# Performance work log

Measured on AMD Instinct MI355X. Metric: run time of the kernel, lower is better.

Reference implementation:

```python
import jax, jax.numpy as jnp
import numpy as np

N_NODES = 100000
N_EDGES = 1600000
F_IN = 128
HID = 128
N_GRAPHS = 64
G_FEAT = 16
N_CLASSES = 10


def _segment_softmax(e, seg, n):
    # numerically stable softmax over edges grouped by target node
    m = jax.ops.segment_max(e, seg, num_segments=n)
    ex = jnp.exp(e - m[seg])
    s = jax.ops.segment_sum(ex, seg, num_segments=n)
    return ex / s[seg]


def _gat_layer(x, src, dst, W, a_src, a_dst, b, n):
    # PyG GATConv (1 head): h = xW; e_ij = LeakyReLU(a_src.h_j + a_dst.h_i)
    h = x @ W                               # [N, H]
    es = h @ a_src                          # [N]
    ed = h @ a_dst                          # [N]
    e = jax.nn.leaky_relu(es[src] + ed[dst], negative_slope=0.2)  # [E]
    alpha = _segment_softmax(e, dst, n)     # softmax over incoming edges
    out = jax.ops.segment_sum(h[src] * alpha[:, None], dst, num_segments=n)
    return out + b


def setup_inputs() -> dict:
    key = jax.random.key(0)
    ks = jax.random.split(key, 16)
    x = jax.random.normal(ks[0], (N_NODES, F_IN), dtype=jnp.float32)
    edge_index = jax.random.randint(ks[1], (2, N_EDGES), 0, N_NODES)
    batch = jnp.sort(jax.random.randint(ks[2], (N_NODES,), 0, N_GRAPHS))
    graph_features = jax.random.normal(ks[3], (N_GRAPHS, G_FEAT), dtype=jnp.float32)
    s1 = 1.0 / np.sqrt(F_IN)
    s2 = 1.0 / np.sqrt(HID)
    params = dict(
        W1=jax.random.uniform(ks[4], (F_IN, HID), minval=-s1, maxval=s1),
        as1=jax.random.uniform(ks[5], (HID,), minval=-s2, maxval=s2),
        ad1=jax.random.uniform(ks[6], (HID,), minval=-s2, maxval=s2),
        b1=jnp.zeros((HID,), jnp.float32),
        W2=jax.random.uniform(ks[7], (HID, HID), minval=-s2, maxval=s2),
        as2=jax.random.uniform(ks[8], (HID,), minval=-s2, maxval=s2),
        ad2=jax.random.uniform(ks[9], (HID,), minval=-s2, maxval=s2),
        b2=jnp.zeros((HID,), jnp.float32),
        linW=jax.random.uniform(ks[10], (HID + G_FEAT, N_CLASSES), minval=-s2, maxval=s2),
        linb=jnp.zeros((N_CLASSES,), jnp.float32),
    )
    return dict(x=x, edge_index=edge_index, batch=batch,
                graph_features=graph_features, **params)


def reference(x, edge_index, batch, graph_features,
              W1, as1, ad1, b1, W2, as2, ad2, b2, linW, linb):
    n = x.shape[0]
    # add self loops (PyG GATConv default add_self_loops=True)
    loops = jnp.arange(n, dtype=edge_index.dtype)
    src = jnp.concatenate([edge_index[0], loops])
    dst = jnp.concatenate([edge_index[1], loops])

    h = jax.nn.relu(_gat_layer(x, src, dst, W1, as1, ad1, b1, n))
    h = jax.nn.relu(_gat_layer(h, src, dst, W2, as2, ad2, b2, n))

    # global_mean_pool over batch segments
    sums = jax.ops.segment_sum(h, batch, num_segments=N_GRAPHS)
    cnt = jax.ops.segment_sum(jnp.ones((n,), h.dtype), batch, num_segments=N_GRAPHS)
    pooled = sums / jnp.maximum(cnt, 1.0)[:, None]      # [G, H]
    # dropout(p=0.5) is identity at inference
    feat = jnp.concatenate([pooled, graph_features], axis=1)  # [G, H+G_FEAT]
    return feat @ linW + linb                           # [G, num_classes]
```

## Files before the change

kernel.cpp:

```cpp
#include <hip/hip_runtime.h>

#define WAVE 64
#define BUCKET_CAP 5632
#define NBUF 400
#define EPB 4096
#define PCHUNK 32

typedef __attribute__((ext_vector_type(8))) short short8v;
typedef __attribute__((ext_vector_type(4))) float floatx4;
typedef __attribute__((ext_vector_type(2))) float floatx2;

__device__ __forceinline__ ushort f2bf(float f) {
    union { float f; unsigned u; } v; v.f = f;
    unsigned r = v.u + 0x7FFF + ((v.u >> 16) & 1);
    return (ushort)(r >> 16);
}
__device__ __forceinline__ float bf2f(ushort u) {
    union { unsigned u; float f; } v; v.u = ((unsigned)u) << 16;
    return v.f;
}


__global__ void k_init(int* __restrict__ zreg, int nzero, int zblocks,
                       const float* __restrict__ W1, const float* __restrict__ W2,
                       ushort* __restrict__ T1, ushort* __restrict__ T2) {
    int b = blockIdx.x;
    if (b < zblocks) {
        int i = b * 256 + threadIdx.x;
        if (i < nzero) zreg[i] = 0;
    } else {
        const float* W = (b == zblocks) ? W1 : W2;
        ushort* T = (b == zblocks) ? T1 : T2;
        for (int i = threadIdx.x; i < 16384; i += 256) {
            int k = i >> 7, n = i & 127;
            T[n * 128 + k] = f2bf(W[k * 128 + n]);
        }
    }
}


__global__ __launch_bounds__(256) void k_bucket(const int* __restrict__ src,
                                                const int* __restrict__ dst,
                                                int E, int N, int B,
                                                int* __restrict__ bcnt,
                                                int* __restrict__ bucket) {
    __shared__ int cnt[NBUF];
    __shared__ int gbase[NBUF];
    int t = threadIdx.x;
    long base = (long)blockIdx.x * EPB;

    for (int k = t; k < NBUF; k += 256) cnt[k] = 0;
    __syncthreads();

    int pay[16], bk[16];
#pragma unroll
    for (int k = 0; k < 16; ++k) {
        long i = base + (long)k * 256 + t;
        bk[k] = -1;
        if (i < (long)E + N) {
            int d, s;
            if (i < E) { d = dst[i]; s = src[i]; }
            else       { d = (int)(i - E); s = d; }
            int b = d >> 8;
            bk[k] = b;
            pay[k] = ((d & 255) << 17) | s;
            atomicAdd(&cnt[b], 1);
        }
    }
    __syncthreads();

    for (int k = t; k < NBUF; k += 256) {
        int c = cnt[k];
        gbase[k] = (c > 0 && k < B) ? atomicAdd(&bcnt[k], c) : 0;
        cnt[k] = 0;
    }
    __syncthreads();

#pragma unroll
    for (int k = 0; k < 16; ++k) {
        if (bk[k] >= 0) {
            int lpos = atomicAdd(&cnt[bk[k]], 1);
            int pos = gbase[bk[k]] + lpos;
            if (pos < BUCKET_CAP)
                bucket[(size_t)bk[k] * BUCKET_CAP + pos] = pay[k];
        }
    }
}

__global__ void k_bscan(const int* __restrict__ bcnt, int* __restrict__ bbase,
                        int B, int Etot, int* __restrict__ offs, int N) {
    __shared__ int sh[512];
    int t = threadIdx.x;
    int v = (t < B) ? bcnt[t] : 0;
    sh[t] = v;
    __syncthreads();
    for (int o = 1; o < 512; o <<= 1) {
        int u = (t >= o) ? sh[t - o] : 0;
        __syncthreads();
        sh[t] += u;
        __syncthreads();
    }
    if (t < B) bbase[t] = sh[t] - v;
    if (t == 0) offs[N] = Etot;
}

__global__ __launch_bounds__(256) void k_csr(const int* __restrict__ bcnt,
                                             const int* __restrict__ bbase,
                                             const int* __restrict__ bucket,
                                             int* __restrict__ offs,
                                             int* __restrict__ csr, int N) {
    __shared__ int ebuf[BUCKET_CAP];
    __shared__ int cnt[256], sc[256], cur[256];
    int b = blockIdx.x, t = threadIdx.x;
    int n = bcnt[b]; if (n > BUCKET_CAP) n = BUCKET_CAP;
    int base = bbase[b];
    cnt[t] = 0;
    __syncthreads();
    const int* bk = bucket + (size_t)b * BUCKET_CAP;
    for (int k = t; k < n; k += 256) {
        int e = bk[k];
        ebuf[k] = e;
        atomicAdd(&cnt[e >> 17], 1);
    }
    __syncthreads();
    sc[t] = cnt[t];
    __syncthreads();
    for (int o = 1; o < 256; o <<= 1) {
        int u = (t >= o) ? sc[t - o] : 0;
        __syncthreads();
        sc[t] += u;
        __syncthreads();
    }
    int loff = sc[t] - cnt[t];
    int node = (b << 8) + t;
    if (node < N) offs[node] = base + loff;
    cur[t] = loff;
    __syncthreads();
    for (int k = t; k < n; k += 256) {
        int e = ebuf[k];
        int pos = base + atomicAdd(&cur[e >> 17], 1);
        csr[pos] = e & 0x1FFFF;
    }
}


template<bool AF32>
__global__ __launch_bounds__(256) void k_gemm_mfma(const void* __restrict__ Ain,
                                                   const ushort* __restrict__ Wt,
                                                   const float* __restrict__ a_s,
                                                   const float* __restrict__ a_d,
                                                   unsigned char* __restrict__ Cf8,
                                                   float* __restrict__ es,
                                                   float* __restrict__ ed, int M) {
    __shared__ ushort As[64][128];
    __shared__ ushort Ws[128][128];
    int t = threadIdx.x;
    int lane = t & 63, wid = t >> 6;
    int row0 = blockIdx.x * 64;

    {
        short8v w[8];
#pragma unroll
        for (int it = 0; it < 8; ++it) {
            int idx = it * 256 + t;
            w[it] = *(const short8v*)&Wt[(idx >> 4) * 128 + (idx & 15) * 8];
        }
#pragma unroll
        for (int it = 0; it < 8; ++it) {
            int idx = it * 256 + t;
            int r = idx >> 4, ch = idx & 15;
            *(short8v*)&Ws[r][(ch ^ (r & 15)) * 8] = w[it];
        }
    }
    {
        short8v a[4];
#pragma unroll
        for (int it = 0; it < 4; ++it) {
            int idx = it * 256 + t;
            int r = idx >> 4, ch = idx & 15;
            int gr = row0 + r;
            short8v u = {0, 0, 0, 0, 0, 0, 0, 0};
            if (gr < M) {
                if (AF32) {
                    const float* A = (const float*)Ain;
                    float4 f0 = *(const float4*)&A[(size_t)gr * 128 + ch * 8];
                    float4 f1 = *(const float4*)&A[(size_t)gr * 128 + ch * 8 + 4];
                    u[0] = (short)f2bf(f0.x); u[1] = (short)f2bf(f0.y);
                    u[2] = (short)f2bf(f0.z); u[3] = (short)f2bf(f0.w);
                    u[4] = (short)f2bf(f1.x); u[5] = (short)f2bf(f1.y);
                    u[6] = (short)f2bf(f1.z); u[7] = (short)f2bf(f1.w);
                } else {
                    const ushort* A = (const ushort*)Ain;
                    u = *(const short8v*)&A[(size_t)gr * 128 + ch * 8];
                }
            }
            a[it] = u;
        }
#pragma unroll
        for (int it = 0; it < 4; ++it) {
            int idx = it * 256 + t;
            int r = idx >> 4, ch = idx & 15;
            *(short8v*)&As[r][(ch ^ (r & 15)) * 8] = a[it];
        }
    }
    __syncthreads();

    int mrow = wid * 16;
    int col = lane & 15;
    int kg = lane >> 4;
    floatx4 acc[8] = {};

#pragma unroll
    for (int ks = 0; ks < 4; ++ks) {
        int chb = ks * 4 + kg;
        int r0 = mrow + col;
        short8v a0 = *(short8v*)&As[r0][(chb ^ (r0 & 15)) * 8];
        short8v b[8];
#pragma unroll
        for (int ni = 0; ni < 8; ++ni) {
            int rn = ni * 16 + col;
            b[ni] = *(short8v*)&Ws[rn][(chb ^ (rn & 15)) * 8];
        }
#pragma unroll
        for (int ni = 0; ni < 8; ++ni)
            acc[ni] = __builtin_amdgcn_mfma_f32_16x16x32_bf16(b[ni], a0, acc[ni], 0, 0, 0);
    }

    int node = row0 + mrow + col;
    bool ok = node < M;
    float esp = 0.f, edp = 0.f;
#pragma unroll
    for (int ni = 0; ni < 8; ++ni) {
        floatx4 v = acc[ni];
        float4 sv = *(const float4*)(a_s + ni * 16 + kg * 4);
        float4 dv = *(const float4*)(a_d + ni * 16 + kg * 4);
        esp += v[0] * sv.x + v[1] * sv.y + v[2] * sv.z + v[3] * sv.w;
        edp += v[0] * dv.x + v[1] * dv.y + v[2] * dv.z + v[3] * dv.w;
        int lo = __builtin_amdgcn_cvt_pk_fp8_f32(v[0], v[1], 0, false);
        int dw = __builtin_amdgcn_cvt_pk_fp8_f32(v[2], v[3], lo, true);
        if (ok) *(int*)&Cf8[(size_t)node * 128 + ni * 16 + kg * 4] = dw;
    }
    esp += __shfl_xor(esp, 16); esp += __shfl_xor(esp, 32);
    edp += __shfl_xor(edp, 16); edp += __shfl_xor(edp, 32);
    if (ok && kg == 0) { es[node] = esp; ed[node] = edp; }
}


__global__ __launch_bounds__(256) void k_aggregate(const unsigned char* __restrict__ hf8,
                                                   const float* __restrict__ es,
                                                   const float* __restrict__ ed,
                                                   const int* __restrict__ csr_src,
                                                   const int* __restrict__ offs,
                                                   const float* __restrict__ bias,
                                                   ushort* __restrict__ out, int N) {
    __shared__ __align__(16) float2 pe[4][64];
    int wid  = threadIdx.x >> 6;
    int lane = threadIdx.x & 63;
    int w = (blockIdx.x * 256 + threadIdx.x) >> 6;
    if (w >= N) return;
    int beg = offs[w], end = offs[w + 1];
    float edi = ed[w];
    int grp = lane >> 4, fc = lane & 15;
    const unsigned char* hbase = hf8 + fc * 8;

    float s_lane = 0.f;
    float acc[8] = {0.f, 0.f, 0.f, 0.f, 0.f, 0.f, 0.f, 0.f};

    for (int tb = beg; tb < end; tb += WAVE) {
        int cnt = end - tb; if (cnt > WAVE) cnt = WAVE;

        float p = 0.f;
        int sj = 0;
        if (lane < cnt) {
            sj = csr_src[tb + lane];
            float t = es[sj] + edi;
            float e = (t > 0.f) ? t : 0.2f * t;
            p = __expf(e);
        }
        s_lane += p;
        pe[wid][lane] = make_float2(p, __int_as_float(sj << 7));
        asm volatile("s_waitcnt lgkmcnt(0)" ::: "memory");

        __builtin_amdgcn_s_setprio(1);
        int cnt4 = (cnt + 3) & ~3;
        for (int k = 0; k < cnt4; k += 4) {
            float2 pr = pe[wid][k + grp];
            float p_ = pr.x;
            int off = __float_as_int(pr.y);
            uint2 v = *(const uint2*)(hbase + off);
            floatx2 f0 = __builtin_amdgcn_cvt_pk_f32_fp8(v.x, false);
            floatx2 f1 = __builtin_amdgcn_cvt_pk_f32_fp8(v.x, true);
            floatx2 f2 = __builtin_amdgcn_cvt_pk_f32_fp8(v.y, false);
            floatx2 f3 = __builtin_amdgcn_cvt_pk_f32_fp8(v.y, true);
            acc[0] += p_ * f0.x; acc[1] += p_ * f0.y;
            acc[2] += p_ * f1.x; acc[3] += p_ * f1.y;
            acc[4] += p_ * f2.x; acc[5] += p_ * f2.y;
            acc[6] += p_ * f3.x; acc[7] += p_ * f3.y;
        }
        __builtin_amdgcn_s_setprio(0);
    }

    float s = s_lane;
#pragma unroll
    for (int o = 32; o; o >>= 1) s += __shfl_xor(s, o);

#pragma unroll
    for (int i = 0; i < 8; ++i) {
        acc[i] += __shfl_xor(acc[i], 16);
        acc[i] += __shfl_xor(acc[i], 32);
    }

    if (grp == 0) {
        float rinv = 1.f / s;
        float4 b0 = *(const float4*)(bias + fc * 8);
        float4 b1 = *(const float4*)(bias + fc * 8 + 4);
        float o_[8];
        o_[0] = fmaxf(acc[0] * rinv + b0.x, 0.f);
        o_[1] = fmaxf(acc[1] * rinv + b0.y, 0.f);
        o_[2] = fmaxf(acc[2] * rinv + b0.z, 0.f);
        o_[3] = fmaxf(acc[3] * rinv + b0.w, 0.f);
        o_[4] = fmaxf(acc[4] * rinv + b1.x, 0.f);
        o_[5] = fmaxf(acc[5] * rinv + b1.y, 0.f);
        o_[6] = fmaxf(acc[6] * rinv + b1.z, 0.f);
        o_[7] = fmaxf(acc[7] * rinv + b1.w, 0.f);
        uint4 pk;
        pk.x = (unsigned)f2bf(o_[0]) | ((unsigned)f2bf(o_[1]) << 16);
        pk.y = (unsigned)f2bf(o_[2]) | ((unsigned)f2bf(o_[3]) << 16);
        pk.z = (unsigned)f2bf(o_[4]) | ((unsigned)f2bf(o_[5]) << 16);
        pk.w = (unsigned)f2bf(o_[6]) | ((unsigned)f2bf(o_[7]) << 16);
        *(uint4*)(out + (size_t)w * 128 + fc * 8) = pk;
    }
}


__global__ __launch_bounds__(128) void k_poolsum(const ushort* __restrict__ h,
                                                 const int* __restrict__ batch,
                                                 float* __restrict__ sums,
                                                 int* __restrict__ cnt, int N) {
    int t = threadIdx.x;
    int base = blockIdx.x * PCHUNK;
    if (base >= N) return;

    int cur = batch[base];
    float acc = 0.f;
    int cnum = 0;

    if (base + PCHUNK <= N) {
#pragma unroll
        for (int k = 0; k < PCHUNK; ++k) {
            int i = base + k;
            int g = batch[i];
            float v = bf2f(h[(size_t)i * 128 + t]);
            if (g != cur) {
                atomicAdd(&sums[cur * 128 + t], acc);
                if (t == 0) atomicAdd(&cnt[cur], cnum);
                acc = 0.f; cnum = 0; cur = g;
            }
            acc += v;
            ++cnum;
        }
    } else {
        for (int i = base; i < N; ++i) {
            int g = batch[i];
            float v = bf2f(h[(size_t)i * 128 + t]);
            if (g != cur) {
                atomicAdd(&sums[cur * 128 + t], acc);
                if (t == 0) atomicAdd(&cnt[cur], cnum);
                acc = 0.f; cnum = 0; cur = g;
            }
            acc += v;
            ++cnum;
        }
    }
    atomicAdd(&sums[cur * 128 + t], acc);
    if (t == 0) atomicAdd(&cnt[cur], cnum);
}

__global__ __launch_bounds__(64) void k_head(const float* __restrict__ sums,
                                             const int* __restrict__ cnt,
                                             const float* __restrict__ gf,
                                             const float* __restrict__ linW,
                                             const float* __restrict__ linb,
                                             float* __restrict__ out) {
    int g = blockIdx.x, t = threadIdx.x;
    __shared__ float feat[144];
    float c = fmaxf((float)cnt[g], 1.f);
    for (int k = t; k < 128; k += 64) feat[k] = sums[g * 128 + k] / c;
    if (t < 16) feat[128 + t] = gf[g * 16 + t];
    __syncthreads();
    if (t < 10) {
        float acc = linb[t];
        for (int k = 0; k < 144; ++k) acc += feat[k] * linW[k * 10 + t];
        out[g * 10 + t] = acc;
    }
}


extern "C" void kernel_launch(void* const* d_in, const int* in_sizes, int n_in,
                              void* d_out, int out_size, void* d_ws, size_t ws_size,
                              hipStream_t stream) {
    const float* x    = (const float*)d_in[0];
    const int*   eidx = (const int*)d_in[1];
    const int*   batch = (const int*)d_in[2];
    const float* gf   = (const float*)d_in[3];
    const float* W1   = (const float*)d_in[4];
    const float* as1  = (const float*)d_in[5];
    const float* ad1  = (const float*)d_in[6];
    const float* b1   = (const float*)d_in[7];
    const float* W2   = (const float*)d_in[8];
    const float* as2  = (const float*)d_in[9];
    const float* ad2  = (const float*)d_in[10];
    const float* b2   = (const float*)d_in[11];
    const float* linW = (const float*)d_in[12];
    const float* linb = (const float*)d_in[13];
    float* out = (float*)d_out;

    const int N = in_sizes[0] / 128;
    const int E = in_sizes[1] / 2;
    const int Etot = E + N;
    const int B = (N + 255) >> 8;
    const int* srcp = eidx;
    const int* dstp = eidx + E;

    char* ws = (char*)d_ws;
    size_t off = 0;
    auto alloc = [&](size_t bytes) -> void* {
        void* p = ws + off;
        off += (bytes + 255) & ~(size_t)255;
        return p;
    };
    unsigned char* hAf8 = (unsigned char*)alloc((size_t)N * 128);
    ushort* hBb   = (ushort*)alloc((size_t)N * 128 * 2);
    float*  esed  = (float*)alloc((size_t)2 * N * 4);
    float*  es = esed, *ed = esed + N;
    ushort* Wt1   = (ushort*)alloc(16384 * 2);
    ushort* Wt2   = (ushort*)alloc(16384 * 2);
    int*    offs  = (int*)alloc((size_t)(N + 1) * 4);
    int*    bbase = (int*)alloc((size_t)B * 4);
    int*    bucket= (int*)alloc((size_t)B * BUCKET_CAP * 4);
    int*    csr   = (int*)alloc((size_t)Etot * 4);
    int nzero = B + 64 * 128 + 64;
    int*    zreg  = (int*)alloc((size_t)nzero * 4);
    int*    bcnt  = zreg;
    float*  psums = (float*)(zreg + B);
    int*    pcnt  = zreg + B + 64 * 128;

    int zblocks = (nzero + 255) / 256;
    k_init<<<zblocks + 2, 256, 0, stream>>>(zreg, nzero, zblocks, W1, W2, Wt1, Wt2);

    k_bucket<<<(Etot + EPB - 1) / EPB, 256, 0, stream>>>(srcp, dstp, E, N, B, bcnt, bucket);
    k_bscan<<<1, 512, 0, stream>>>(bcnt, bbase, B, Etot, offs, N);
    k_csr<<<B, 256, 0, stream>>>(bcnt, bbase, bucket, offs, csr, N);

    int gblocks = (N + 63) / 64;
    int wblocks = ((size_t)N * 64 + 255) / 256;

    k_gemm_mfma<true><<<gblocks, 256, 0, stream>>>(x, Wt1, as1, ad1, hAf8, es, ed, N);
    k_aggregate<<<wblocks, 256, 0, stream>>>(hAf8, es, ed, csr, offs, b1, hBb, N);

    k_gemm_mfma<false><<<gblocks, 256, 0, stream>>>(hBb, Wt2, as2, ad2, hAf8, es, ed, N);
    k_aggregate<<<wblocks, 256, 0, stream>>>(hAf8, es, ed, csr, offs, b2, hBb, N);

    k_poolsum<<<(N + PCHUNK - 1) / PCHUNK, 128, 0, stream>>>(hBb, batch, psums, pcnt, N);
    k_head<<<64, 64, 0, stream>>>(psums, pcnt, gf, linW, linb, out);
}
```

Measured before the change: 244.1 us.

## Fuse mean-pool sum into final aggregation and derive graph counts by binary search

The second-layer aggregation kernel now accumulates its ReLU outputs directly into per-graph pooled sums: a block-level shared-memory reduction handles nodes in the block's first graph, with global atomics for the rest. This removes the bf16 write of the final hidden layer, the separate pooling kernel and its reread. The head kernel computes node counts per graph by binary search over the sorted batch array instead of atomic counters. The cost is more shared and global atomics inside the aggregation epilogue and extra barriers in a memory-bound kernel.

```diff
diff --git a/kernel.cpp b/kernel.cpp
--- a/kernel.cpp
+++ b/kernel.cpp
@@ -4,7 +4,6 @@
 #define BUCKET_CAP 5632
 #define NBUF 400
 #define EPB 4096
-#define PCHUNK 32
 
 typedef __attribute__((ext_vector_type(8))) short short8v;
 typedef __attribute__((ext_vector_type(4))) float floatx4;
@@ -246,20 +245,35 @@
 }
 
 
+template<bool FINAL>
 __global__ __launch_bounds__(256) void k_aggregate(const unsigned char* __restrict__ hf8,
                                                    const float* __restrict__ es,
                                                    const float* __restrict__ ed,
                                                    const int* __restrict__ csr_src,
                                                    const int* __restrict__ offs,
                                                    const float* __restrict__ bias,
-                                                   ushort* __restrict__ out, int N) {
+                                                   ushort* __restrict__ out,
+                                                   const int* __restrict__ batch,
+                                                   float* __restrict__ psums, int N) {
     __shared__ __align__(16) float2 pe[4][64];
-    int wid  = threadIdx.x >> 6;
-    int lane = threadIdx.x & 63;
-    int w = (blockIdx.x * 256 + threadIdx.x) >> 6;
-    if (w >= N) return;
-    int beg = offs[w], end = offs[w + 1];
-    float edi = ed[w];
+    __shared__ float bsum[128];
+    __shared__ int g0s;
+    int tid = threadIdx.x;
+    int wid  = tid >> 6;
+    int lane = tid & 63;
+    int w = (blockIdx.x * 256 + tid) >> 6;
+    bool active = w < N;
+    if (!FINAL && !active) return;
+
+    if (FINAL) {
+        for (int i = tid; i < 128; i += 256) bsum[i] = 0.f;
+        if (tid == 0) g0s = batch[blockIdx.x * 4 < N ? blockIdx.x * 4 : N - 1];
+        __syncthreads();
+    }
+
+    int beg = 0, end = 0;
+    float edi = 0.f;
+    if (active) { beg = offs[w]; end = offs[w + 1]; edi = ed[w]; }
     int grp = lane >> 4, fc = lane & 15;
     const unsigned char* hbase = hf8 + fc * 8;
 
@@ -310,11 +324,12 @@
         acc[i] += __shfl_xor(acc[i], 32);
     }
 
-    if (grp == 0) {
+    float o_[8];
+    bool emit = (grp == 0) && active;
+    if (emit) {
         float rinv = 1.f / s;
         float4 b0 = *(const float4*)(bias + fc * 8);
         float4 b1 = *(const float4*)(bias + fc * 8 + 4);
-        float o_[8];
         o_[0] = fmaxf(acc[0] * rinv + b0.x, 0.f);
         o_[1] = fmaxf(acc[1] * rinv + b0.y, 0.f);
         o_[2] = fmaxf(acc[2] * rinv + b0.z, 0.f);
@@ -323,68 +338,49 @@
         o_[5] = fmaxf(acc[5] * rinv + b1.y, 0.f);
         o_[6] = fmaxf(acc[6] * rinv + b1.z, 0.f);
         o_[7] = fmaxf(acc[7] * rinv + b1.w, 0.f);
-        uint4 pk;
-        pk.x = (unsigned)f2bf(o_[0]) | ((unsigned)f2bf(o_[1]) << 16);
-        pk.y = (unsigned)f2bf(o_[2]) | ((unsigned)f2bf(o_[3]) << 16);
-        pk.z = (unsigned)f2bf(o_[4]) | ((unsigned)f2bf(o_[5]) << 16);
-        pk.w = (unsigned)f2bf(o_[6]) | ((unsigned)f2bf(o_[7]) << 16);
-        *(uint4*)(out + (size_t)w * 128 + fc * 8) = pk;
-    }
-}
-
-
-__global__ __launch_bounds__(128) void k_poolsum(const ushort* __restrict__ h,
-                                                 const int* __restrict__ batch,
-                                                 float* __restrict__ sums,
-                                                 int* __restrict__ cnt, int N) {
-    int t = threadIdx.x;
-    int base = blockIdx.x * PCHUNK;
-    if (base >= N) return;
-
-    int cur = batch[base];
-    float acc = 0.f;
-    int cnum = 0;
-
-    if (base + PCHUNK <= N) {
-#pragma unroll
-        for (int k = 0; k < PCHUNK; ++k) {
-            int i = base + k;
-            int g = batch[i];
-            float v = bf2f(h[(size_t)i * 128 + t]);
-            if (g != cur) {
-                atomicAdd(&sums[cur * 128 + t], acc);
-                if (t == 0) atomicAdd(&cnt[cur], cnum);
-                acc = 0.f; cnum = 0; cur = g;
+    }
+
+    if (!FINAL) {
+        if (emit) {
+            uint4 pk;
+            pk.x = (unsigned)f2bf(o_[0]) | ((unsigned)f2bf(o_[1]) << 16);
+            pk.y = (unsigned)f2bf(o_[2]) | ((unsigned)f2bf(o_[3]) << 16);
+            pk.z = (unsigned)f2bf(o_[4]) | ((unsigned)f2bf(o_[5]) << 16);
+            pk.w = (unsigned)f2bf(o_[6]) | ((unsigned)f2bf(o_[7]) << 16);
+            *(uint4*)(out + (size_t)w * 128 + fc * 8) = pk;
+        }
+    } else {
+        if (emit) {
+            int g = batch[w];
+            if (g == g0s) {
+#pragma unroll
+                for (int i = 0; i < 8; ++i) atomicAdd(&bsum[fc * 8 + i], o_[i]);
+            } else {
+#pragma unroll
+                for (int i = 0; i < 8; ++i) atomicAdd(&psums[g * 128 + fc * 8 + i], o_[i]);
             }
-            acc += v;
-            ++cnum;
-        }
-    } else {
-        for (int i = base; i < N; ++i) {
-            int g = batch[i];
-            float v = bf2f(h[(size_t)i * 128 + t]);
-            if (g != cur) {
-                atomicAdd(&sums[cur * 128 + t], acc);
-                if (t == 0) atomicAdd(&cnt[cur], cnum);
-                acc = 0.f; cnum = 0; cur = g;
-            }
-            acc += v;
-            ++cnum;
-        }
-    }
-    atomicAdd(&sums[cur * 128 + t], acc);
-    if (t == 0) atomicAdd(&cnt[cur], cnum);
-}
+        }
+        __syncthreads();
+        if (tid < 128) {
+            float v = bsum[tid];
+            if (v != 0.f) atomicAdd(&psums[g0s * 128 + tid], v);
+        }
+    }
+}
+
 
 __global__ __launch_bounds__(64) void k_head(const float* __restrict__ sums,
-                                             const int* __restrict__ cnt,
+                                             const int* __restrict__ batch,
                                              const float* __restrict__ gf,
                                              const float* __restrict__ linW,
                                              const float* __restrict__ linb,
-                                             float* __restrict__ out) {
+                                             float* __restrict__ out, int N) {
     int g = blockIdx.x, t = threadIdx.x;
     __shared__ float feat[144];
-    float c = fmaxf((float)cnt[g], 1.f);
+    int lo, hi;
+    { int a = 0, b = N; while (a < b) { int mid = (a + b) >> 1; if (batch[mid] < g) a = mid + 1; else b = mid; } lo = a; }
+    { int a = lo, b = N; while (a < b) { int mid = (a + b) >> 1; if (batch[mid] < g + 1) a = mid + 1; else b = mid; } hi = a; }
+    float c = fmaxf((float)(hi - lo), 1.f);
     for (int k = t; k < 128; k += 64) feat[k] = sums[g * 128 + k] / c;
     if (t < 16) feat[128 + t] = gf[g * 16 + t];
     __syncthreads();
@@ -439,11 +435,10 @@
     int*    bbase = (int*)alloc((size_t)B * 4);
     int*    bucket= (int*)alloc((size_t)B * BUCKET_CAP * 4);
     int*    csr   = (int*)alloc((size_t)Etot * 4);
-    int nzero = B + 64 * 128 + 64;
+    int nzero = B + 64 * 128;
     int*    zreg  = (int*)alloc((size_t)nzero * 4);
     int*    bcnt  = zreg;
     float*  psums = (float*)(zreg + B);
-    int*    pcnt  = zreg + B + 64 * 128;
 
     int zblocks = (nzero + 255) / 256;
     k_init<<<zblocks + 2, 256, 0, stream>>>(zreg, nzero, zblocks, W1, W2, Wt1, Wt2);
@@ -456,11 +451,12 @@
     int wblocks = ((size_t)N * 64 + 255) / 256;
 
     k_gemm_mfma<true><<<gblocks, 256, 0, stream>>>(x, Wt1, as1, ad1, hAf8, es, ed, N);
-    k_aggregate<<<wblocks, 256, 0, stream>>>(hAf8, es, ed, csr, offs, b1, hBb, N);
+    k_aggregate<false><<<wblocks, 256, 0, stream>>>(hAf8, es, ed, csr, offs, b1, hBb,
+                                                    batch, psums, N);
 
     k_gemm_mfma<false><<<gblocks, 256, 0, stream>>>(hBb, Wt2, as2, ad2, hAf8, es, ed, N);
-    k_aggregate<<<wblocks, 256, 0, stream>>>(hAf8, es, ed, csr, offs, b2, hBb, N);
-
-    k_poolsum<<<(N + PCHUNK - 1) / PCHUNK, 128, 0, stream>>>(hBb, batch, psums, pcnt, N);
-    k_head<<<64, 64, 0, stream>>>(psums, pcnt, gf, linW, linb, out);
-}
+    k_aggregate<true><<<wblocks, 256, 0, stream>>>(hAf8, es, ed, csr, offs, b2, nullptr,
+                                                   batch, psums, N);
+
+    k_head<<<64, 64, 0, stream>>>(psums, batch, gf, linW, linb, out, N);
+}
```

New measurement: 305.9 us. 25.3% more time.
